# Kernel tuning notes

Measured on AMD Instinct MI355X. Metric: run time of the kernel, lower is better.

## Reference

```python
import jax, jax.numpy as jnp
import numpy as np

R = 16            # search_range
D = 2 * R + 1     # 33 offsets per axis -> 1089 cost channels
B, C, H, W = 64, 256, 16, 16
OUT = 512         # conv channels for search_range=16
FULLY = 1024
EPS_BN = 1e-5
EPS_NORM = 1e-12
LRELU_SLOPE = 0.01


def l2_normalize(x):
    # torch F.normalize(x, dim=1, p=2): x / clamp_min(||x||_2, 1e-12)
    n = jnp.sqrt(jnp.sum(x * x, axis=1, keepdims=True))
    return x / jnp.maximum(n, EPS_NORM)


def cost_volume(c1, warp, r):
    # Fused equivalent of the original (2r+1)^2 Python-loop of slice/mul/mean:
    # one dense correlation GEMM over the padded map, then a gather of the
    # diagonal-band entries. cost[b,dy,dx,i,j] = mean_c c1[b,c,i,j]*pad[b,c,i+dy,j+dx]
    b, c, h, w = c1.shape
    d = 2 * r + 1
    padded = jnp.pad(warp, ((0, 0), (0, 0), (r, r), (r, r)))          # (B,C,h+2r,w+2r)
    full = jnp.einsum('bcij,bcuv->bijuv', c1, padded) / c             # (B,h,w,h+2r,w+2r)
    dy = jnp.arange(d)
    ii = jnp.arange(h)
    jj = jnp.arange(w)
    I = ii[None, None, :, None]                 # (1,1,h,1)
    J = jj[None, None, None, :]                 # (1,1,1,w)
    U = dy[:, None, None, None] + I             # (d,1,h,1)
    V = dy[None, :, None, None] + J             # (1,d,1,w)
    cost = full[:, I, J, U, V]                  # (B,d,d,h,w)
    cost = cost.reshape(b, d * d, h, w)
    return jnp.where(cost > 0, cost, LRELU_SLOPE * cost)  # LeakyReLU(0.01)


def conv_bn_relu(x, Wc, bc, g, be, stride):
    y = jax.lax.conv_general_dilated(
        x, Wc, window_strides=(stride, stride), padding=((1, 1), (1, 1)),
        dimension_numbers=('NCHW', 'OIHW', 'NCHW'))
    y = y + bc[None, :, None, None]
    # training-mode BatchNorm: biased batch stats over (B,H,W)
    mu = jnp.mean(y, axis=(0, 2, 3), keepdims=True)
    var = jnp.var(y, axis=(0, 2, 3), keepdims=True)
    y = (y - mu) * jax.lax.rsqrt(var + EPS_BN)
    y = y * g[None, :, None, None] + be[None, :, None, None]
    return jnp.maximum(y, 0.0)


def setup_inputs() -> dict:
    key = jax.random.key(0)
    ks = jax.random.split(key, 10)
    s = 0.02
    inp = {
        'feature1': jax.random.normal(ks[0], (B, C, H, W), jnp.float32),
        'feature2': jax.random.normal(ks[1], (B, C, H, W), jnp.float32),
        'W1': jax.random.normal(ks[2], (OUT, D * D, 3, 3), jnp.float32) * s,
        'b1': jnp.zeros((OUT,), jnp.float32),
        'g1': jnp.ones((OUT,), jnp.float32),
        'be1': jnp.zeros((OUT,), jnp.float32),
        'W2': jax.random.normal(ks[3], (OUT, OUT, 3, 3), jnp.float32) * s,
        'b2': jnp.zeros((OUT,), jnp.float32),
        'g2': jnp.ones((OUT,), jnp.float32),
        'be2': jnp.zeros((OUT,), jnp.float32),
        'W3': jax.random.normal(ks[4], (OUT, OUT, 3, 3), jnp.float32) * s,
        'b3': jnp.zeros((OUT,), jnp.float32),
        'g3': jnp.ones((OUT,), jnp.float32),
        'be3': jnp.zeros((OUT,), jnp.float32),
        'Wf1': jax.random.normal(ks[5], (FULLY, 256 * OUT), jnp.float32) * s,
        'bf1': jnp.zeros((FULLY,), jnp.float32),
        'Wf2': jax.random.normal(ks[6], (8, FULLY), jnp.float32) * s,
        'bf2': jnp.zeros((8,), jnp.float32),
    }
    return inp


def reference(feature1, feature2, W1, b1, g1, be1, W2, b2, g2, be2,
              W3, b3, g3, be3, Wf1, bf1, Wf2, bf2):
    # warped=False: normalize both feature maps
    gc = cost_volume(l2_normalize(feature1), l2_normalize(feature2), R)
    x = conv_bn_relu(gc, W1, b1, g1, be1, 1)
    x = conv_bn_relu(x, W2, b2, g2, be2, 1)
    x = conv_bn_relu(x, W3, b3, g3, be3, 1)
    x = x.reshape(x.shape[0], -1)               # (B, 512*16*16)
    x = jnp.maximum(x @ Wf1.T + bf1, 0.0)       # Linear + ReLU
    # Dropout treated as identity (deterministic reference)
    offset = x @ Wf2.T + bf2                    # (B, 8)
    return offset
```

## Files before the change

### kernel.cpp

```cpp
#include <hip/hip_runtime.h>
#include <hip/hip_bf16.h>
#include <stdint.h>


typedef unsigned short ushort_t;
typedef __attribute__((ext_vector_type(8))) short     bf16x8;
typedef __attribute__((ext_vector_type(8))) unsigned short u16x8;
typedef __attribute__((ext_vector_type(4))) unsigned short u16x4;
typedef __attribute__((ext_vector_type(2))) unsigned short u16x2;
typedef __attribute__((ext_vector_type(4))) float     f32x4;

#define NB   64
#define NC   256
#define NP   256
#define KP1  1152
#define NOUT 512
#define NROWS 16384
#define KFC  131072
#define NF   1024
#define KSPL 32

__device__ __forceinline__ unsigned short f2bf(float x) {
  union { float f; unsigned u; } c; c.f = x;
  unsigned r = c.u + 0x7FFFu + ((c.u >> 16) & 1u);
  return (unsigned short)(r >> 16);
}
__device__ __forceinline__ float b2f(unsigned short u) {
  union { unsigned u; float f; } c; c.u = ((unsigned)u) << 16; return c.f;
}

__device__ __forceinline__ void gl_lds16(const void* g, void* l) {
  __builtin_amdgcn_global_load_lds(
      (const __attribute__((address_space(1))) unsigned int*)g,
      (__attribute__((address_space(3))) unsigned int*)l, 16, 0, 0);
}

__device__ __forceinline__ f32x4 mfma16(bf16x8 a, bf16x8 b, f32x4 c) {
  return __builtin_amdgcn_mfma_f32_16x16x32_bf16(a, b, c, 0, 0, 0);
}

__global__ __launch_bounds__(256) void l2norm_t(
    const float* __restrict__ f1, const float* __restrict__ f2,
    ushort_t* __restrict__ AT, ushort_t* __restrict__ N2T)
{
  const float* src = blockIdx.y ? f2 : f1;
  ushort_t*    dst = blockIdx.y ? N2T : AT;
  const int b = blockIdx.x, t = threadIdx.x;
  const float* sb = src + (size_t)b * NC * NP;
  float sq = 0.f;
  for (int c = 0; c < NC; ++c) { float v = sb[c * NP + t]; sq += v * v; }
  float sc = 1.f / fmaxf(sqrtf(sq), 1e-12f);
  ushort_t* db = dst + ((size_t)b * NP + t) * NC;
  for (int c0 = 0; c0 < NC; c0 += 8) {
    u16x8 pk;
#pragma unroll
    for (int q = 0; q < 8; ++q) pk[q] = f2bf(sb[(c0 + q) * NP + t] * sc);
    *(u16x8*)(db + c0) = pk;
  }
}

#define T1P (9 * NOUT * KP1)
#define T23 (9 * NOUT * 512)
__global__ __launch_bounds__(256) void pack_all(
    const float* __restrict__ W1, const float* __restrict__ W2,
    const float* __restrict__ W3, ushort_t* __restrict__ Wp1,
    ushort_t* __restrict__ Wp2, ushort_t* __restrict__ Wp3)
{
  int p = blockIdx.x * 256 + threadIdx.x;
  const float* W; ushort_t* Wp; int Cin, Kp, q;
  if (p < T1P)            { W = W1; Wp = Wp1; Cin = 1089; Kp = KP1; q = p; }
  else if (p < T1P + T23) { W = W2; Wp = Wp2; Cin = 512;  Kp = 512; q = p - T1P; }
  else if (p < T1P + 2 * T23) { W = W3; Wp = Wp3; Cin = 512; Kp = 512; q = p - T1P - T23; }
  else return;
  int tap = q / (NOUT * Kp);
  int rem = q - tap * (NOUT * Kp);
  int o   = rem / Kp;
  int cin = rem - o * Kp;
  float v = (cin < Cin) ? W[((size_t)o * Cin + cin) * 9 + tap] : 0.f;
  Wp[q] = f2bf(v);
}

__global__ __launch_bounds__(256) void corr_gemm(
    const ushort_t* __restrict__ AT,
    const ushort_t* __restrict__ N2T,
    float* __restrict__ C)
{
  __shared__ ushort_t As[128 * 64];
  __shared__ ushort_t Bs[128 * 64];
  const int tid = threadIdx.x, lane = tid & 63, wave = tid >> 6;
  const int wr = wave >> 1, wc = wave & 1;
  const int la = lane & 15, lb = lane >> 4;
  const int b  = blockIdx.z;
  const int m0 = blockIdx.y * 128;
  const int n0 = blockIdx.x * 128;

  f32x4 acc[4][4];
#pragma unroll
  for (int i = 0; i < 4; ++i)
#pragma unroll
    for (int j = 0; j < 4; ++j) acc[i][j] = (f32x4){0.f, 0.f, 0.f, 0.f};

  const ushort_t* srcA[4];
  const ushort_t* srcB[4];
#pragma unroll
  for (int s = 0; s < 4; ++s) {
    int idx = tid + (s << 8);
    int row = idx >> 3, c16 = idx & 7;
    srcA[s] = AT  + ((size_t)b * NP + m0 + row) * NC + c16 * 8;
    srcB[s] = N2T + ((size_t)b * NP + n0 + row) * NC + c16 * 8;
  }

  for (int kc = 0; kc < NC; kc += 64) {
#pragma unroll
    for (int s = 0; s < 4; ++s) {
      int idx = tid + (s << 8);
      gl_lds16(srcA[s] + kc, &As[idx * 8]);
      gl_lds16(srcB[s] + kc, &Bs[idx * 8]);
    }
    __syncthreads();
#pragma unroll
    for (int kk = 0; kk < 2; ++kk) {
      bf16x8 af[4], bfv[4];
#pragma unroll
      for (int mi = 0; mi < 4; ++mi)
        af[mi] = *(const bf16x8*)&As[(wr * 64 + mi * 16 + la) * 64 + kk * 32 + lb * 8];
#pragma unroll
      for (int ni = 0; ni < 4; ++ni)
        bfv[ni] = *(const bf16x8*)&Bs[(wc * 64 + ni * 16 + la) * 64 + kk * 32 + lb * 8];
#pragma unroll
      for (int mi = 0; mi < 4; ++mi)
#pragma unroll
        for (int ni = 0; ni < 4; ++ni)
          acc[mi][ni] = mfma16(af[mi], bfv[ni], acc[mi][ni]);
    }
    __syncthreads();
  }

#pragma unroll
  for (int ni = 0; ni < 4; ++ni) {
    int col = n0 + wc * 64 + ni * 16 + la;
#pragma unroll
    for (int mi = 0; mi < 4; ++mi) {
      int p = m0 + wr * 64 + mi * 16 + lb * 4;
#pragma unroll
      for (int r = 0; r < 4; ++r)
        C[((size_t)b * NP + p + r) * NP + col] = acc[mi][ni][r];
    }
  }
}

__global__ __launch_bounds__(576) void cost_write(
    const float* __restrict__ C, ushort_t* __restrict__ costT)
{
  __shared__ float row[256];
  const int ij = blockIdx.x, b = blockIdx.y, tid = threadIdx.x;
  const float* cr = C + ((size_t)b * NP + ij) * NP;
  if (tid < 256) row[tid] = cr[tid];
  __syncthreads();
  const int i = ij >> 4, j = ij & 15;
  const int d0 = tid * 2;
  u16x2 pk;
#pragma unroll
  for (int q = 0; q < 2; ++q) {
    int dd = d0 + q;
    int dy = dd / 33;
    int dx = dd - dy * 33;
    int oi = dy + i - 16, oj = dx + j - 16;
    float v = 0.f;
    if (((unsigned)oi < 16u) & ((unsigned)oj < 16u))
      v = row[oi * 16 + oj] * (1.f / 256.f);
    v = v > 0.f ? v : 0.01f * v;
    pk[q] = f2bf(v);
  }
  *(u16x2*)(costT + ((size_t)b * NP + ij) * KP1 + d0) = pk;
}

__global__ __launch_bounds__(512, 1) void conv_gemm256(
    const ushort_t* __restrict__ X, const ushort_t* __restrict__ Wp,
    const float* __restrict__ bias, ushort_t* __restrict__ Y0,
    ushort_t* __restrict__ Y1, const int K, const int TPT, const int NT2,
    const ushort_t* __restrict__ zerot)
{
  __shared__ ushort_t lds[65536];
  const int tid = threadIdx.x;
  const int lane = tid & 63, wave = tid >> 6;
  const int wr = wave >> 2, wc = wave & 3;
  const int la = lane & 15, lb = lane >> 4;

  const int bid = blockIdx.x;
  const int L = ((bid & 7) << 5) + (bid >> 3);
  const int g = L >> 7;
  const int rem = L & 127;
  const int b = rem >> 1;
  const int n0 = (rem & 1) << 8;
  const int t0 = g * NT2;

  int amask[4];
  const ushort_t* abase[4];
  const ushort_t* bbase[4];
#pragma unroll
  for (int s = 0; s < 4; ++s) {
    int idx = tid + (s << 9);
    int ks = idx & 7, loc = (idx >> 3) & 63;
    int rA = ((s & 1) << 7) + ((s >> 1) << 6) + loc;
    int i = rA >> 4, j = rA & 15;
    int m = 0;
#pragma unroll
    for (int tap = 0; tap < 9; ++tap) {
      int i2 = i + tap / 3 - 1, j2 = j + tap % 3 - 1;
      if (((unsigned)i2 < 16u) & ((unsigned)j2 < 16u)) m |= 1 << tap;
    }
    amask[s] = m;
    abase[s] = X + (size_t)(b * NP + rA) * K + ((ks ^ (rA & 7)) << 3);
    int rB = ((s & 1) << 7) + ((loc >> 5) << 6) + ((s >> 1) << 5) + (loc & 31);
    bbase[s] = Wp + (size_t)(n0 + rB) * K + ((ks ^ (rB & 7)) << 3);
  }

  const int ck0 = ((0 + lb) ^ (la & 7)) << 3;
  const int ck1 = ((4 + lb) ^ (la & 7)) << 3;
  const int a_base = wr * 4096 + la * 64;
  const int b_base = 16384 + (wc >> 1) * 4096 + (wc & 1) * 2048 + la * 64;

  f32x4 acc[8][4];
#pragma unroll
  for (int i = 0; i < 8; ++i)
#pragma unroll
    for (int j = 0; j < 4; ++j) acc[i][j] = (f32x4){0.f, 0.f, 0.f, 0.f};

  auto tile_par = [&](int tg, int& toffA, size_t& wtap, int& tap) {
    tap = tg / TPT;
    int kc = (tg - tap * TPT) << 6;
    int ty = tap / 3;
    toffA = (ty * 16 + (tap - 3 * ty) - 17) * K + kc;
    wtap  = (size_t)tap * NOUT * K + kc;
  };

#define STAGE_A(S) { const ushort_t* gp = ((amask[S] >> tapN) & 1) ? abase[S] + toffN : zerot; \
                     gl_lds16(gp, &bufn[(tid + ((S) << 9)) * 8]); }
#define STAGE_B(S) gl_lds16(bbase[S] + wtapN, &bufn[16384 + (tid + ((S) << 9)) * 8]);

#define READ_A03() \
  Af[0][0] = *(const bf16x8*)&buf[a_base + 0    + ck0]; Af[0][1] = *(const bf16x8*)&buf[a_base + 0    + ck1]; \
  Af[1][0] = *(const bf16x8*)&buf[a_base + 1024 + ck0]; Af[1][1] = *(const bf16x8*)&buf[a_base + 1024 + ck1]; \
  Af[2][0] = *(const bf16x8*)&buf[a_base + 2048 + ck0]; Af[2][1] = *(const bf16x8*)&buf[a_base + 2048 + ck1]; \
  Af[3][0] = *(const bf16x8*)&buf[a_base + 3072 + ck0]; Af[3][1] = *(const bf16x8*)&buf[a_base + 3072 + ck1];
#define READ_A47() \
  Af[4][0] = *(const bf16x8*)&buf[a_base + 8192 + 0    + ck0]; Af[4][1] = *(const bf16x8*)&buf[a_base + 8192 + 0    + ck1]; \
  Af[5][0] = *(const bf16x8*)&buf[a_base + 8192 + 1024 + ck0]; Af[5][1] = *(const bf16x8*)&buf[a_base + 8192 + 1024 + ck1]; \
  Af[6][0] = *(const bf16x8*)&buf[a_base + 8192 + 2048 + ck0]; Af[6][1] = *(const bf16x8*)&buf[a_base + 8192 + 2048 + ck1]; \
  Af[7][0] = *(const bf16x8*)&buf[a_base + 8192 + 3072 + ck0]; Af[7][1] = *(const bf16x8*)&buf[a_base + 8192 + 3072 + ck1];
#define READ_B(NOFF) \
  bf00 = *(const bf16x8*)&buf[b_base + (NOFF) + 0    + ck0]; bf01 = *(const bf16x8*)&buf[b_base + (NOFF) + 0    + ck1]; \
  bf10 = *(const bf16x8*)&buf[b_base + (NOFF) + 1024 + ck0]; bf11 = *(const bf16x8*)&buf[b_base + (NOFF) + 1024 + ck1];
#define MFMA_QUAD(MB, N0, N1) \
  acc[MB+0][N0] = mfma16(Af[MB+0][0], bf00, acc[MB+0][N0]); \
  acc[MB+0][N1] = mfma16(Af[MB+0][0], bf10, acc[MB+0][N1]); \
  acc[MB+1][N0] = mfma16(Af[MB+1][0], bf00, acc[MB+1][N0]); \
  acc[MB+1][N1] = mfma16(Af[MB+1][0], bf10, acc[MB+1][N1]); \
  acc[MB+2][N0] = mfma16(Af[MB+2][0], bf00, acc[MB+2][N0]); \
  acc[MB+2][N1] = mfma16(Af[MB+2][0], bf10, acc[MB+2][N1]); \
  acc[MB+3][N0] = mfma16(Af[MB+3][0], bf00, acc[MB+3][N0]); \
  acc[MB+3][N1] = mfma16(Af[MB+3][0], bf10, acc[MB+3][N1]); \
  acc[MB+0][N0] = mfma16(Af[MB+0][1], bf01, acc[MB+0][N0]); \
  acc[MB+0][N1] = mfma16(Af[MB+0][1], bf11, acc[MB+0][N1]); \
  acc[MB+1][N0] = mfma16(Af[MB+1][1], bf01, acc[MB+1][N0]); \
  acc[MB+1][N1] = mfma16(Af[MB+1][1], bf11, acc[MB+1][N1]); \
  acc[MB+2][N0] = mfma16(Af[MB+2][1], bf01, acc[MB+2][N0]); \
  acc[MB+2][N1] = mfma16(Af[MB+2][1], bf11, acc[MB+2][N1]); \
  acc[MB+3][N0] = mfma16(Af[MB+3][1], bf01, acc[MB+3][N0]); \
  acc[MB+3][N1] = mfma16(Af[MB+3][1], bf11, acc[MB+3][N1]);

  {
    ushort_t* bufn = &lds[0];
    int tapN, toffN; size_t wtapN;
    tile_par(t0, toffN, wtapN, tapN);
    STAGE_A(0) STAGE_A(1) STAGE_A(2) STAGE_A(3)
    STAGE_B(0) STAGE_B(1) STAGE_B(2) STAGE_B(3)
  }
  asm volatile("s_waitcnt vmcnt(2)" ::: "memory");
  __builtin_amdgcn_s_barrier();

  bf16x8 Af[8][2];

  for (int t = 0; t < NT2 - 1; ++t) {
    const ushort_t* buf = &lds[(t & 1) << 15];
    ushort_t* bufn = &lds[((t + 1) & 1) << 15];
    int tapN, toffN; size_t wtapN;
    tile_par(t0 + t + 1, toffN, wtapN, tapN);
    bf16x8 bf00, bf01, bf10, bf11;

    READ_A03()
    READ_B(0)
    STAGE_A(0) STAGE_A(1)
    asm volatile("s_waitcnt vmcnt(6)" ::: "memory");
    __builtin_amdgcn_s_barrier();
    asm volatile("s_waitcnt lgkmcnt(0)" ::: "memory");
    __builtin_amdgcn_sched_barrier(0);
    __builtin_amdgcn_s_setprio(1);
    MFMA_QUAD(0, 0, 1)
    __builtin_amdgcn_s_setprio(0);

    READ_A47()
    READ_B(0)
    STAGE_A(2) STAGE_A(3)
    asm volatile("s_waitcnt vmcnt(4)" ::: "memory");
    __builtin_amdgcn_s_barrier();
    asm volatile("s_waitcnt lgkmcnt(0)" ::: "memory");
    __builtin_amdgcn_sched_barrier(0);
    __builtin_amdgcn_s_setprio(1);
    MFMA_QUAD(4, 0, 1)
    __builtin_amdgcn_s_setprio(0);

    READ_B(8192)
    STAGE_B(0) STAGE_B(1)
    __builtin_amdgcn_s_barrier();
    asm volatile("s_waitcnt lgkmcnt(0)" ::: "memory");
    __builtin_amdgcn_sched_barrier(0);
    __builtin_amdgcn_s_setprio(1);
    MFMA_QUAD(0, 2, 3)
    __builtin_amdgcn_s_setprio(0);

    READ_B(8192)
    STAGE_B(2) STAGE_B(3)
    asm volatile("s_waitcnt vmcnt(2)" ::: "memory");
    __builtin_amdgcn_s_barrier();
    asm volatile("s_waitcnt lgkmcnt(0)" ::: "memory");
    __builtin_amdgcn_sched_barrier(0);
    __builtin_amdgcn_s_setprio(1);
    MFMA_QUAD(4, 2, 3)
    __builtin_amdgcn_s_setprio(0);
  }

  {
    const ushort_t* buf = &lds[((NT2 - 1) & 1) << 15];
    bf16x8 bf00, bf01, bf10, bf11;
    asm volatile("s_waitcnt vmcnt(0)" ::: "memory");
    __builtin_amdgcn_s_barrier();
    READ_A03()
    READ_B(0)
    asm volatile("s_waitcnt lgkmcnt(0)" ::: "memory");
    __builtin_amdgcn_sched_barrier(0);
    MFMA_QUAD(0, 0, 1)
    READ_A47()
    asm volatile("s_waitcnt lgkmcnt(0)" ::: "memory");
    __builtin_amdgcn_sched_barrier(0);
    MFMA_QUAD(4, 0, 1)
    READ_B(8192)
    asm volatile("s_waitcnt lgkmcnt(0)" ::: "memory");
    __builtin_amdgcn_sched_barrier(0);
    MFMA_QUAD(0, 2, 3)
    MFMA_QUAD(4, 2, 3)
  }

  ushort_t* Yh = g ? Y1 : Y0;
#pragma unroll
  for (int ni = 0; ni < 4; ++ni) {
    int col = n0 + wc * 64 + ni * 16 + la;
    float bv = 0.5f * bias[col];
#pragma unroll
    for (int mi = 0; mi < 8; ++mi) {
      int row = b * NP + wr * 128 + mi * 16 + lb * 4;
#pragma unroll
      for (int r = 0; r < 4; ++r)
        Yh[(size_t)(row + r) * NOUT + col] = f2bf(acc[mi][ni][r] + bv);
    }
  }
#undef STAGE_A
#undef STAGE_B
#undef READ_A03
#undef READ_A47
#undef READ_B
#undef MFMA_QUAD
}

__global__ __launch_bounds__(512) void bn_stat2(
    const ushort_t* __restrict__ Y0, const ushort_t* __restrict__ Y1,
    float* __restrict__ st)
{
  const int col = threadIdx.x;
  const size_t base = (size_t)blockIdx.x * 32 * NOUT;
  float s = 0.f, q = 0.f;
  for (int r = 0; r < 32; ++r) {
    float y = b2f(Y0[base + r * NOUT + col]) + b2f(Y1[base + r * NOUT + col]);
    s += y; q += y * y;
  }
  atomicAdd(&st[col], s);
  atomicAdd(&st[512 + col], q);
}

__global__ __launch_bounds__(256) void bn_apply2(
    const ushort_t* __restrict__ Y0, const ushort_t* __restrict__ Y1,
    const float* __restrict__ st, const float* __restrict__ g,
    const float* __restrict__ be, ushort_t* __restrict__ Xo)
{
  const size_t idx = (size_t)blockIdx.x * 256 + threadIdx.x;
  u16x8 a = *(const u16x8*)(Y0 + idx * 8);
  u16x8 c = *(const u16x8*)(Y1 + idx * 8);
  const int c0 = (int)((idx * 8) & 511);
  u16x8 pk;
#pragma unroll
  for (int q = 0; q < 8; ++q) {
    int cc = c0 + q;
    float y = b2f(a[q]) + b2f(c[q]);
    float mu  = st[cc] * (1.f / 16384.f);
    float var = st[512 + cc] * (1.f / 16384.f) - mu * mu;
    float s = rsqrtf(var + 1e-5f) * g[cc];
    pk[q] = f2bf(fmaxf((y - mu) * s + be[cc], 0.f));
  }
  *(u16x8*)(Xo + idx * 8) = pk;
}

__global__ __launch_bounds__(256) void bn_apply2_t(
    const ushort_t* __restrict__ Y0, const ushort_t* __restrict__ Y1,
    const float* __restrict__ st, const float* __restrict__ g,
    const float* __restrict__ be, ushort_t* __restrict__ Xf)
{
  __shared__ ushort_t T[64][65];
  const int c0  = blockIdx.x * 64;
  const int ij0 = blockIdx.y * 64;
  const int b   = blockIdx.z;
  const int tid = threadIdx.x;

#pragma unroll
  for (int it = 0; it < 16; ++it) {
    int e = it * 256 + tid;
    int ij = e >> 6, c = e & 63;
    int cg = c0 + c;
    size_t off = ((size_t)(b * NP + ij0 + ij)) * NOUT + cg;
    float y = b2f(Y0[off]) + b2f(Y1[off]);
    float mu  = st[cg] * (1.f / 16384.f);
    float var = st[512 + cg] * (1.f / 16384.f) - mu * mu;
    float s = rsqrtf(var + 1e-5f) * g[cg];
    T[ij][c] = f2bf(fmaxf((y - mu) * s + be[cg], 0.f));
  }
  __syncthreads();
#pragma unroll
  for (int it = 0; it < 16; ++it) {
    int e = it * 256 + tid;
    int cr = e >> 6, ijc = e & 63;
    Xf[(size_t)b * KFC + (size_t)(c0 + cr) * NP + ij0 + ijc] = T[ijc][cr];
  }
}

__device__ __forceinline__ u16x8 pack8(float4 a, float4 b) {
  u16x8 r;
  r[0] = f2bf(a.x); r[1] = f2bf(a.y); r[2] = f2bf(a.z); r[3] = f2bf(a.w);
  r[4] = f2bf(b.x); r[5] = f2bf(b.y); r[6] = f2bf(b.z); r[7] = f2bf(b.w);
  return r;
}

__global__ __launch_bounds__(256) void fc1_gemm(
    const ushort_t* __restrict__ Xf, const float* __restrict__ Wf1,
    float* __restrict__ hacc)
{
  __shared__ ushort_t As[64 * 64];
  __shared__ ushort_t Bs[64 * 64];
  const int tid = threadIdx.x, lane = tid & 63, wave = tid >> 6;
  const int la = lane & 15, lb = lane >> 4;
  const int f0 = blockIdx.x * 64;
  const int k0 = blockIdx.y * 4096;

  f32x4 acc[4];
#pragma unroll
  for (int i = 0; i < 4; ++i) acc[i] = (f32x4){0.f, 0.f, 0.f, 0.f};

  const ushort_t* xrow[2];
#pragma unroll
  for (int s = 0; s < 2; ++s) {
    int idx = tid + (s << 8);
    xrow[s] = Xf + (size_t)(idx >> 3) * KFC + k0 + (idx & 7) * 8;
  }
  const int brow = tid >> 2, kseg = (tid & 3) * 16;
  const float* wrow = Wf1 + (size_t)(f0 + brow) * KFC + k0 + kseg;

  for (int kc = 0; kc < 4096; kc += 64) {
#pragma unroll
    for (int s = 0; s < 2; ++s) {
      int idx = tid + (s << 8);
      gl_lds16(xrow[s] + kc, &As[idx * 8]);
    }
    float4 w0 = *(const float4*)(wrow + kc);
    float4 w1 = *(const float4*)(wrow + kc + 4);
    float4 w2 = *(const float4*)(wrow + kc + 8);
    float4 w3 = *(const float4*)(wrow + kc + 12);
    *(u16x8*)&Bs[brow * 64 + kseg]     = pack8(w0, w1);
    *(u16x8*)&Bs[brow * 64 + kseg + 8] = pack8(w2, w3);
    __syncthreads();
#pragma unroll
    for (int kk = 0; kk < 2; ++kk) {
      bf16x8 bfv = *(const bf16x8*)&Bs[(wave * 16 + la) * 64 + kk * 32 + lb * 8];
#pragma unroll
      for (int mi = 0; mi < 4; ++mi) {
        bf16x8 av = *(const bf16x8*)&As[(mi * 16 + la) * 64 + kk * 32 + lb * 8];
        acc[mi] = mfma16(av, bfv, acc[mi]);
      }
    }
    __syncthreads();
  }

  float* slice = hacc + (size_t)blockIdx.y * NB * NF;
#pragma unroll
  for (int mi = 0; mi < 4; ++mi) {
    int row = mi * 16 + lb * 4;
#pragma unroll
    for (int r = 0; r < 4; ++r)
      slice[(size_t)(row + r) * NF + f0 + wave * 16 + la] = acc[mi][r];
  }
}

__global__ __launch_bounds__(256) void fc2_out(
    const float* __restrict__ hacc, const float* __restrict__ bf1,
    const float* __restrict__ Wf2, const float* __restrict__ bf2,
    float* __restrict__ out)
{
  const int b = blockIdx.x, tid = threadIdx.x;
  float a[8];
#pragma unroll
  for (int o = 0; o < 8; ++o) a[o] = 0.f;
  for (int f = tid; f < NF; f += 256) {
    float hv = bf1[f];
#pragma unroll 4
    for (int s = 0; s < KSPL; ++s)
      hv += hacc[((size_t)s * NB + b) * NF + f];
    hv = fmaxf(hv, 0.f);
#pragma unroll
    for (int o = 0; o < 8; ++o) a[o] += hv * Wf2[o * NF + f];
  }
  __shared__ float red[8][256];
#pragma unroll
  for (int o = 0; o < 8; ++o) red[o][tid] = a[o];
  __syncthreads();
  for (int s = 128; s > 0; s >>= 1) {
    if (tid < s) {
#pragma unroll
      for (int o = 0; o < 8; ++o) red[o][tid] += red[o][tid + s];
    }
    __syncthreads();
  }
  if (tid < 8) out[b * 8 + tid] = red[tid][0] + bf2[tid];
}

extern "C" void kernel_launch(void* const* d_in, const int* in_sizes, int n_in,
                              void* d_out, int out_size, void* d_ws, size_t ws_size,
                              hipStream_t stream) {
  const float* f1  = (const float*)d_in[0];
  const float* f2  = (const float*)d_in[1];
  const float* W1  = (const float*)d_in[2];
  const float* b1  = (const float*)d_in[3];
  const float* g1  = (const float*)d_in[4];
  const float* be1 = (const float*)d_in[5];
  const float* W2  = (const float*)d_in[6];
  const float* b2  = (const float*)d_in[7];
  const float* g2  = (const float*)d_in[8];
  const float* be2 = (const float*)d_in[9];
  const float* W3  = (const float*)d_in[10];
  const float* b3  = (const float*)d_in[11];
  const float* g3  = (const float*)d_in[12];
  const float* be3 = (const float*)d_in[13];
  const float* Wf1 = (const float*)d_in[14];
  const float* bf1 = (const float*)d_in[15];
  const float* Wf2 = (const float*)d_in[16];
  const float* bf2 = (const float*)d_in[17];
  float* out = (float*)d_out;

  char* ws = (char*)d_ws;
  size_t off = 0;
  auto alloc = [&](size_t bytes) -> void* {
    void* p = ws + off;
    off += (bytes + 255) & ~(size_t)255;
    return p;
  };

  ushort_t* zerot = (ushort_t*)alloc(256);
  float* st1  = (float*)alloc(1024 * 4);
  float* st2  = (float*)alloc(1024 * 4);
  float* st3  = (float*)alloc(1024 * 4);
  const size_t zero_bytes = off;

  float* hacc = (float*)alloc((size_t)KSPL * NB * NF * 4);
  const size_t SZ_AT   = (size_t)NB * NP * NC * 2;
  const size_t SZ_COST = (size_t)NB * NP * KP1 * 2;
  const size_t SZ_WP1  = (size_t)9 * NOUT * KP1 * 2;
  const size_t SZ_WP23 = (size_t)9 * NOUT * 512 * 2;
  ushort_t* AT    = (ushort_t*)alloc(SZ_AT);
  ushort_t* N2T   = (ushort_t*)alloc(SZ_AT);
  float*    Cbuf  = (float*)alloc((size_t)NB * NP * NP * 4);
  ushort_t* costT = (ushort_t*)alloc(SZ_COST);
  ushort_t* Wp1   = (ushort_t*)alloc(SZ_WP1);
  ushort_t* Wp2   = (ushort_t*)alloc(SZ_WP23);
  ushort_t* Wp3   = (ushort_t*)alloc(SZ_WP23);
  ushort_t* Yh0   = (ushort_t*)alloc((size_t)NROWS * NOUT * 2);
  ushort_t* Yh1   = (ushort_t*)alloc((size_t)NROWS * NOUT * 2);
  ushort_t* Xbuf  = (ushort_t*)alloc((size_t)NROWS * NOUT * 2);
  ushort_t* Xf    = (ushort_t*)alloc((size_t)NB * KFC * 2);

  hipMemsetAsync(ws, 0, zero_bytes, stream);

  l2norm_t<<<dim3(64, 2), 256, 0, stream>>>(f1, f2, AT, N2T);

  pack_all<<<(T1P + 2 * T23 + 255) / 256, 256, 0, stream>>>(W1, W2, W3, Wp1, Wp2, Wp3);

  corr_gemm<<<dim3(2, 2, 64), 256, 0, stream>>>(AT, N2T, Cbuf);
  cost_write<<<dim3(256, 64), 576, 0, stream>>>(Cbuf, costT);

  conv_gemm256<<<256, 512, 0, stream>>>(costT, Wp1, b1, Yh0, Yh1, KP1, 18, 81, zerot);
  bn_stat2<<<512, 512, 0, stream>>>(Yh0, Yh1, st1);
  bn_apply2<<<4096, 256, 0, stream>>>(Yh0, Yh1, st1, g1, be1, Xbuf);

  conv_gemm256<<<256, 512, 0, stream>>>(Xbuf, Wp2, b2, Yh0, Yh1, 512, 8, 36, zerot);
  bn_stat2<<<512, 512, 0, stream>>>(Yh0, Yh1, st2);
  bn_apply2<<<4096, 256, 0, stream>>>(Yh0, Yh1, st2, g2, be2, Xbuf);

  conv_gemm256<<<256, 512, 0, stream>>>(Xbuf, Wp3, b3, Yh0, Yh1, 512, 8, 36, zerot);
  bn_stat2<<<512, 512, 0, stream>>>(Yh0, Yh1, st3);
  bn_apply2_t<<<dim3(8, 4, 64), 256, 0, stream>>>(Yh0, Yh1, st3, g3, be3, Xf);

  fc1_gemm<<<dim3(16, KSPL), 256, 0, stream>>>(Xf, Wf1, hacc);
  fc2_out<<<64, 256, 0, stream>>>(hacc, bf1, Wf2, bf2, out);

  (void)in_sizes; (void)n_in; (void)out_size; (void)ws_size;
}
```

Baseline: 607.3 us.

## Fuse BN statistics into conv2/conv3 GEMM epilogue and drop split-K partials

Adds conv_fused, a 256x128-tile conv GEMM without split-K. It writes a single bf16 output and accumulates the per-channel sum and sum of squares for BatchNorm in its epilogue with shuffles and atomics. This removes the separate bn_stat2 pass and the second partial-output buffer for layers 2 and 3. The apply kernels are simplified to read one buffer. It also widens l2norm to 1024 threads with an LDS reduction and vectorizes bn_stat2 for layer 1. The cost is fewer blocks per output, each running a longer K loop, and atomic contention on the stats buffers.

```diff
diff --git a/kernel.cpp b/kernel.cpp
--- a/kernel.cpp
+++ b/kernel.cpp
@@ -6,7 +6,6 @@
 typedef unsigned short ushort_t;
 typedef __attribute__((ext_vector_type(8))) short     bf16x8;
 typedef __attribute__((ext_vector_type(8))) unsigned short u16x8;
-typedef __attribute__((ext_vector_type(4))) unsigned short u16x4;
 typedef __attribute__((ext_vector_type(2))) unsigned short u16x2;
 typedef __attribute__((ext_vector_type(4))) float     f32x4;
 
@@ -39,22 +38,31 @@
   return __builtin_amdgcn_mfma_f32_16x16x32_bf16(a, b, c, 0, 0, 0);
 }
 
-__global__ __launch_bounds__(256) void l2norm_t(
+__global__ __launch_bounds__(1024) void l2norm_t(
     const float* __restrict__ f1, const float* __restrict__ f2,
     ushort_t* __restrict__ AT, ushort_t* __restrict__ N2T)
 {
+  __shared__ float red[4][256];
   const float* src = blockIdx.y ? f2 : f1;
   ushort_t*    dst = blockIdx.y ? N2T : AT;
-  const int b = blockIdx.x, t = threadIdx.x;
+  const int b = blockIdx.x;
+  const int pos = threadIdx.x & 255, q = threadIdx.x >> 8;
   const float* sb = src + (size_t)b * NC * NP;
   float sq = 0.f;
-  for (int c = 0; c < NC; ++c) { float v = sb[c * NP + t]; sq += v * v; }
-  float sc = 1.f / fmaxf(sqrtf(sq), 1e-12f);
-  ushort_t* db = dst + ((size_t)b * NP + t) * NC;
-  for (int c0 = 0; c0 < NC; c0 += 8) {
+  for (int c = q * 64; c < q * 64 + 64; ++c) {
+    float v = sb[c * NP + pos]; sq += v * v;
+  }
+  red[q][pos] = sq;
+  __syncthreads();
+  float tot = red[0][pos] + red[1][pos] + red[2][pos] + red[3][pos];
+  float sc = 1.f / fmaxf(sqrtf(tot), 1e-12f);
+  ushort_t* db = dst + ((size_t)b * NP + pos) * NC;
+#pragma unroll
+  for (int j = 0; j < 8; ++j) {
+    int c0 = q * 64 + j * 8;
     u16x8 pk;
 #pragma unroll
-    for (int q = 0; q < 8; ++q) pk[q] = f2bf(sb[(c0 + q) * NP + t] * sc);
+    for (int k = 0; k < 8; ++k) pk[k] = f2bf(sb[(c0 + k) * NP + pos] * sc);
     *(u16x8*)(db + c0) = pk;
   }
 }
@@ -373,19 +381,217 @@
 #undef MFMA_QUAD
 }
 
+__global__ __launch_bounds__(512, 1) void conv_fused(
+    const ushort_t* __restrict__ X, const ushort_t* __restrict__ Wp,
+    const float* __restrict__ bias, ushort_t* __restrict__ Y,
+    float* __restrict__ st, const int K, const int TPT, const int NT,
+    const ushort_t* __restrict__ zerot)
+{
+  __shared__ ushort_t lds[2 * 24576];
+  const int tid = threadIdx.x;
+  const int lane = tid & 63, wave = tid >> 6;
+  const int wr = wave >> 2, wc = wave & 3;
+  const int la = lane & 15, lb = lane >> 4;
+
+  const int bid = blockIdx.x;
+  const int L = ((bid & 7) << 5) + (bid >> 3);
+  const int b = L >> 2;
+  const int n0 = (L & 3) << 7;
+
+  int amask[4];
+  const ushort_t* abase[4];
+  const ushort_t* bbase[2];
+#pragma unroll
+  for (int s = 0; s < 4; ++s) {
+    int idx = tid + (s << 9);
+    int ks = idx & 7, loc = (idx >> 3) & 63;
+    int rA = ((s & 1) << 7) + ((s >> 1) << 6) + loc;
+    int i = rA >> 4, j = rA & 15;
+    int m = 0;
+#pragma unroll
+    for (int tap = 0; tap < 9; ++tap) {
+      int i2 = i + tap / 3 - 1, j2 = j + tap % 3 - 1;
+      if (((unsigned)i2 < 16u) & ((unsigned)j2 < 16u)) m |= 1 << tap;
+    }
+    amask[s] = m;
+    abase[s] = X + (size_t)(b * NP + rA) * K + ((ks ^ (rA & 7)) << 3);
+  }
+#pragma unroll
+  for (int s = 0; s < 2; ++s) {
+    int idx = tid + (s << 9);
+    int ks = idx & 7, loc = (idx >> 3) & 63;
+    int rB = (s << 6) + loc;
+    bbase[s] = Wp + (size_t)(n0 + rB) * K + ((ks ^ (rB & 7)) << 3);
+  }
+
+  const int ck0 = ((0 + lb) ^ (la & 7)) << 3;
+  const int ck1 = ((4 + lb) ^ (la & 7)) << 3;
+  const int a_base = wr * 4096 + la * 64;
+  const int b_off  = 16384 + (wc * 32 + la) * 64;
+
+  f32x4 acc[8][2];
+#pragma unroll
+  for (int i = 0; i < 8; ++i)
+#pragma unroll
+    for (int j = 0; j < 2; ++j) acc[i][j] = (f32x4){0.f, 0.f, 0.f, 0.f};
+
+  auto tile_par = [&](int tg, int& toffA, size_t& wtap, int& tap) {
+    tap = tg / TPT;
+    int kc = (tg - tap * TPT) << 6;
+    int ty = tap / 3;
+    toffA = (ty * 16 + (tap - 3 * ty) - 17) * K + kc;
+    wtap  = (size_t)tap * NOUT * K + kc;
+  };
+
+#define FSTAGE_A(S) { const ushort_t* gp = ((amask[S] >> tapN) & 1) ? abase[S] + toffN : zerot; \
+                      gl_lds16(gp, &bufn[(tid + ((S) << 9)) * 8]); }
+#define FSTAGE_B(S) gl_lds16(bbase[S] + wtapN, &bufn[16384 + (tid + ((S) << 9)) * 8]);
+#define FREAD_A03() \
+  Af[0][0] = *(const bf16x8*)&buf[a_base + 0    + ck0]; Af[0][1] = *(const bf16x8*)&buf[a_base + 0    + ck1]; \
+  Af[1][0] = *(const bf16x8*)&buf[a_base + 1024 + ck0]; Af[1][1] = *(const bf16x8*)&buf[a_base + 1024 + ck1]; \
+  Af[2][0] = *(const bf16x8*)&buf[a_base + 2048 + ck0]; Af[2][1] = *(const bf16x8*)&buf[a_base + 2048 + ck1]; \
+  Af[3][0] = *(const bf16x8*)&buf[a_base + 3072 + ck0]; Af[3][1] = *(const bf16x8*)&buf[a_base + 3072 + ck1];
+#define FREAD_A47() \
+  Af[0][0] = *(const bf16x8*)&buf[a_base + 8192 + 0    + ck0]; Af[0][1] = *(const bf16x8*)&buf[a_base + 8192 + 0    + ck1]; \
+  Af[1][0] = *(const bf16x8*)&buf[a_base + 8192 + 1024 + ck0]; Af[1][1] = *(const bf16x8*)&buf[a_base + 8192 + 1024 + ck1]; \
+  Af[2][0] = *(const bf16x8*)&buf[a_base + 8192 + 2048 + ck0]; Af[2][1] = *(const bf16x8*)&buf[a_base + 8192 + 2048 + ck1]; \
+  Af[3][0] = *(const bf16x8*)&buf[a_base + 8192 + 3072 + ck0]; Af[3][1] = *(const bf16x8*)&buf[a_base + 8192 + 3072 + ck1];
+#define FREAD_B() \
+  Bf[0][0] = *(const bf16x8*)&buf[b_off + 0    + ck0]; Bf[0][1] = *(const bf16x8*)&buf[b_off + 0    + ck1]; \
+  Bf[1][0] = *(const bf16x8*)&buf[b_off + 1024 + ck0]; Bf[1][1] = *(const bf16x8*)&buf[b_off + 1024 + ck1];
+#define FMFMA(AB) \
+  acc[(AB)+0][0] = mfma16(Af[0][0], Bf[0][0], acc[(AB)+0][0]); \
+  acc[(AB)+0][1] = mfma16(Af[0][0], Bf[1][0], acc[(AB)+0][1]); \
+  acc[(AB)+1][0] = mfma16(Af[1][0], Bf[0][0], acc[(AB)+1][0]); \
+  acc[(AB)+1][1] = mfma16(Af[1][0], Bf[1][0], acc[(AB)+1][1]); \
+  acc[(AB)+2][0] = mfma16(Af[2][0], Bf[0][0], acc[(AB)+2][0]); \
+  acc[(AB)+2][1] = mfma16(Af[2][0], Bf[1][0], acc[(AB)+2][1]); \
+  acc[(AB)+3][0] = mfma16(Af[3][0], Bf[0][0], acc[(AB)+3][0]); \
+  acc[(AB)+3][1] = mfma16(Af[3][0], Bf[1][0], acc[(AB)+3][1]); \
+  acc[(AB)+0][0] = mfma16(Af[0][1], Bf[0][1], acc[(AB)+0][0]); \
+  acc[(AB)+0][1] = mfma16(Af[0][1], Bf[1][1], acc[(AB)+0][1]); \
+  acc[(AB)+1][0] = mfma16(Af[1][1], Bf[0][1], acc[(AB)+1][0]); \
+  acc[(AB)+1][1] = mfma16(Af[1][1], Bf[1][1], acc[(AB)+1][1]); \
+  acc[(AB)+2][0] = mfma16(Af[2][1], Bf[0][1], acc[(AB)+2][0]); \
+  acc[(AB)+2][1] = mfma16(Af[2][1], Bf[1][1], acc[(AB)+2][1]); \
+  acc[(AB)+3][0] = mfma16(Af[3][1], Bf[0][1], acc[(AB)+3][0]); \
+  acc[(AB)+3][1] = mfma16(Af[3][1], Bf[1][1], acc[(AB)+3][1]);
+
+  {
+    ushort_t* bufn = &lds[0];
+    int tapN, toffN; size_t wtapN;
+    tile_par(0, toffN, wtapN, tapN);
+    FSTAGE_A(0) FSTAGE_A(1) FSTAGE_B(0) FSTAGE_B(1) FSTAGE_A(2) FSTAGE_A(3)
+  }
+  asm volatile("s_waitcnt vmcnt(2)" ::: "memory");
+  __builtin_amdgcn_s_barrier();
+
+  for (int t = 0; t < NT - 1; ++t) {
+    const ushort_t* buf = &lds[(t & 1) * 24576];
+    ushort_t* bufn = &lds[((t + 1) & 1) * 24576];
+    int tapN, toffN; size_t wtapN;
+    tile_par(t + 1, toffN, wtapN, tapN);
+    bf16x8 Af[4][2], Bf[2][2];
+
+    FREAD_A03()
+    FREAD_B()
+    FSTAGE_A(0) FSTAGE_A(1) FSTAGE_B(0) FSTAGE_B(1)
+    asm volatile("s_waitcnt vmcnt(4)" ::: "memory");
+    __builtin_amdgcn_s_barrier();
+    asm volatile("s_waitcnt lgkmcnt(0)" ::: "memory");
+    __builtin_amdgcn_sched_barrier(0);
+    __builtin_amdgcn_s_setprio(1);
+    FMFMA(0)
+    __builtin_amdgcn_s_setprio(0);
+
+    FREAD_A47()
+    FSTAGE_A(2) FSTAGE_A(3)
+    asm volatile("s_waitcnt vmcnt(2)" ::: "memory");
+    __builtin_amdgcn_s_barrier();
+    asm volatile("s_waitcnt lgkmcnt(0)" ::: "memory");
+    __builtin_amdgcn_sched_barrier(0);
+    __builtin_amdgcn_s_setprio(1);
+    FMFMA(4)
+    __builtin_amdgcn_s_setprio(0);
+  }
+
+  {
+    const ushort_t* buf = &lds[((NT - 1) & 1) * 24576];
+    bf16x8 Af[4][2], Bf[2][2];
+    FREAD_A03()
+    FREAD_B()
+    asm volatile("s_waitcnt vmcnt(0)" ::: "memory");
+    __builtin_amdgcn_s_barrier();
+    asm volatile("s_waitcnt lgkmcnt(0)" ::: "memory");
+    __builtin_amdgcn_sched_barrier(0);
+    FMFMA(0)
+    FREAD_A47()
+    asm volatile("s_waitcnt lgkmcnt(0)" ::: "memory");
+    __builtin_amdgcn_sched_barrier(0);
+    FMFMA(4)
+  }
+
+#pragma unroll
+  for (int ni = 0; ni < 2; ++ni) {
+    int col = n0 + wc * 32 + ni * 16 + la;
+    float bv = bias[col];
+    float s = 0.f, qq = 0.f;
+#pragma unroll
+    for (int mi = 0; mi < 8; ++mi) {
+      int row = b * NP + wr * 128 + mi * 16 + lb * 4;
+#pragma unroll
+      for (int r = 0; r < 4; ++r) {
+        float v = acc[mi][ni][r] + bv;
+        Y[(size_t)(row + r) * NOUT + col] = f2bf(v);
+        s += v; qq += v * v;
+      }
+    }
+    s  += __shfl_xor(s, 16);  s  += __shfl_xor(s, 32);
+    qq += __shfl_xor(qq, 16); qq += __shfl_xor(qq, 32);
+    if (lb == 0) {
+      atomicAdd(&st[col], s);
+      atomicAdd(&st[512 + col], qq);
+    }
+  }
+#undef FSTAGE_A
+#undef FSTAGE_B
+#undef FREAD_A03
+#undef FREAD_A47
+#undef FREAD_B
+#undef FMFMA
+}
+
 __global__ __launch_bounds__(512) void bn_stat2(
     const ushort_t* __restrict__ Y0, const ushort_t* __restrict__ Y1,
     float* __restrict__ st)
 {
-  const int col = threadIdx.x;
+  __shared__ float ls[8][64][8];
+  __shared__ float lq[8][64][8];
+  const int tid = threadIdx.x;
+  const int cg = tid & 63, rr = tid >> 6;
   const size_t base = (size_t)blockIdx.x * 32 * NOUT;
+  float s8[8], q8[8];
+#pragma unroll
+  for (int j = 0; j < 8; ++j) { s8[j] = 0.f; q8[j] = 0.f; }
+  for (int k = 0; k < 4; ++k) {
+    size_t off = base + (size_t)(rr * 4 + k) * NOUT + cg * 8;
+    u16x8 a = *(const u16x8*)(Y0 + off);
+    u16x8 c = *(const u16x8*)(Y1 + off);
+#pragma unroll
+    for (int j = 0; j < 8; ++j) {
+      float y = b2f(a[j]) + b2f(c[j]);
+      s8[j] += y; q8[j] += y * y;
+    }
+  }
+#pragma unroll
+  for (int j = 0; j < 8; ++j) { ls[rr][cg][j] = s8[j]; lq[rr][cg][j] = q8[j]; }
+  __syncthreads();
+  const int cg2 = tid >> 3, j2 = tid & 7;
   float s = 0.f, q = 0.f;
-  for (int r = 0; r < 32; ++r) {
-    float y = b2f(Y0[base + r * NOUT + col]) + b2f(Y1[base + r * NOUT + col]);
-    s += y; q += y * y;
-  }
-  atomicAdd(&st[col], s);
-  atomicAdd(&st[512 + col], q);
+#pragma unroll
+  for (int r = 0; r < 8; ++r) { s += ls[r][cg2][j2]; q += lq[r][cg2][j2]; }
+  atomicAdd(&st[cg2 * 8 + j2], s);
+  atomicAdd(&st[512 + cg2 * 8 + j2], q);
 }
 
 __global__ __launch_bounds__(256) void bn_apply2(
@@ -410,10 +616,31 @@
   *(u16x8*)(Xo + idx * 8) = pk;
 }
 
-__global__ __launch_bounds__(256) void bn_apply2_t(
-    const ushort_t* __restrict__ Y0, const ushort_t* __restrict__ Y1,
-    const float* __restrict__ st, const float* __restrict__ g,
-    const float* __restrict__ be, ushort_t* __restrict__ Xf)
+__global__ __launch_bounds__(256) void bn_apply_s(
+    const ushort_t* __restrict__ Y, const float* __restrict__ st,
+    const float* __restrict__ g, const float* __restrict__ be,
+    ushort_t* __restrict__ Xo)
+{
+  const size_t idx = (size_t)blockIdx.x * 256 + threadIdx.x;
+  u16x8 a = *(const u16x8*)(Y + idx * 8);
+  const int c0 = (int)((idx * 8) & 511);
+  u16x8 pk;
+#pragma unroll
+  for (int q = 0; q < 8; ++q) {
+    int cc = c0 + q;
+    float y = b2f(a[q]);
+    float mu  = st[cc] * (1.f / 16384.f);
+    float var = st[512 + cc] * (1.f / 16384.f) - mu * mu;
+    float s = rsqrtf(var + 1e-5f) * g[cc];
+    pk[q] = f2bf(fmaxf((y - mu) * s + be[cc], 0.f));
+  }
+  *(u16x8*)(Xo + idx * 8) = pk;
+}
+
+__global__ __launch_bounds__(256) void bn_apply_ts(
+    const ushort_t* __restrict__ Y, const float* __restrict__ st,
+    const float* __restrict__ g, const float* __restrict__ be,
+    ushort_t* __restrict__ Xf)
 {
   __shared__ ushort_t T[64][65];
   const int c0  = blockIdx.x * 64;
@@ -426,8 +653,7 @@
     int e = it * 256 + tid;
     int ij = e >> 6, c = e & 63;
     int cg = c0 + c;
-    size_t off = ((size_t)(b * NP + ij0 + ij)) * NOUT + cg;
-    float y = b2f(Y0[off]) + b2f(Y1[off]);
+    float y = b2f(Y[((size_t)(b * NP + ij0 + ij)) * NOUT + cg]);
     float mu  = st[cg] * (1.f / 16384.f);
     float var = st[512 + cg] * (1.f / 16384.f) - mu * mu;
     float s = rsqrtf(var + 1e-5f) * g[cg];
@@ -596,7 +822,7 @@
 
   hipMemsetAsync(ws, 0, zero_bytes, stream);
 
-  l2norm_t<<<dim3(64, 2), 256, 0, stream>>>(f1, f2, AT, N2T);
+  l2norm_t<<<dim3(64, 2), 1024, 0, stream>>>(f1, f2, AT, N2T);
 
   pack_all<<<(T1P + 2 * T23 + 255) / 256, 256, 0, stream>>>(W1, W2, W3, Wp1, Wp2, Wp3);
 
@@ -607,13 +833,11 @@
   bn_stat2<<<512, 512, 0, stream>>>(Yh0, Yh1, st1);
   bn_apply2<<<4096, 256, 0, stream>>>(Yh0, Yh1, st1, g1, be1, Xbuf);
 
-  conv_gemm256<<<256, 512, 0, stream>>>(Xbuf, Wp2, b2, Yh0, Yh1, 512, 8, 36, zerot);
-  bn_stat2<<<512, 512, 0, stream>>>(Yh0, Yh1, st2);
-  bn_apply2<<<4096, 256, 0, stream>>>(Yh0, Yh1, st2, g2, be2, Xbuf);
-
-  conv_gemm256<<<256, 512, 0, stream>>>(Xbuf, Wp3, b3, Yh0, Yh1, 512, 8, 36, zerot);
-  bn_stat2<<<512, 512, 0, stream>>>(Yh0, Yh1, st3);
-  bn_apply2_t<<<dim3(8, 4, 64), 256, 0, stream>>>(Yh0, Yh1, st3, g3, be3, Xf);
+  conv_fused<<<256, 512, 0, stream>>>(Xbuf, Wp2, b2, Yh0, st2, 512, 8, 72, zerot);
+  bn_apply_s<<<4096, 256, 0, stream>>>(Yh0, st2, g2, be2, Xbuf);
+
+  conv_fused<<<256, 512, 0, stream>>>(Xbuf, Wp3, b3, Yh0, st3, 512, 8, 72, zerot);
+  bn_apply_ts<<<dim3(8, 4, 64), 256, 0, stream>>>(Yh0, st3, g3, be3, Xf);
 
   fc1_gemm<<<dim3(16, KSPL), 256, 0, stream>>>(Xf, Wf1, hacc);
   fc2_out<<<64, 256, 0, stream>>>(hacc, bf1, Wf2, bf2, out);
```

Measured after the change: 573.3 us. -5.6%, faster.
